# Optimization experiments

Hardware: AMD Instinct MI355X
Metric: run time of the kernel (lower is better)

The kernel has to match this reference:

```python
import jax, jax.numpy as jnp
import numpy as np

B, N, E = 32, 128, 8192        # graphs, nodes/graph, edges total
IN, ED, H = 64, 32, 128        # node feat, edge feat, hidden
K1, K2, K3 = 64, 32, 16        # ceil(0.5*N) cascade from TopKPooling(ratio=0.5)
EPS = 1e-5


def setup_inputs():
    key = jax.random.key(0)
    ks = jax.random.split(key, 20)
    def rn(i, shape, s=1.0):
        return jax.random.normal(ks[i], shape, dtype=jnp.float32) * s
    x = rn(0, (B * N, IN))
    edge_attr = rn(1, (E, ED))
    epg = E // B  # edges per graph (intra-graph only)
    src = jax.random.randint(ks[2], (B, epg), 0, N)
    dst = jax.random.randint(ks[3], (B, epg), 0, N)
    off = (jnp.arange(B) * N)[:, None]
    edge_index = jnp.stack([(src + off).reshape(-1), (dst + off).reshape(-1)]).astype(jnp.int32)
    batch = jnp.repeat(jnp.arange(B), N).astype(jnp.int32)
    p = {}
    p['nn1_w'] = rn(4, (ED, IN * H), 0.05); p['nn1_b'] = jnp.zeros((IN * H,), jnp.float32)
    p['root1'] = rn(5, (IN, H), 0.1);       p['bias1'] = jnp.zeros((H,), jnp.float32)
    p['nn2_w'] = rn(6, (ED, H * H), 0.05);  p['nn2_b'] = jnp.zeros((H * H,), jnp.float32)
    p['root2'] = rn(7, (H, H), 0.1);        p['bias2'] = jnp.zeros((H,), jnp.float32)
    p['nn3_w'] = rn(8, (ED, H * H), 0.05);  p['nn3_b'] = jnp.zeros((H * H,), jnp.float32)
    p['root3'] = rn(9, (H, H), 0.1);        p['bias3'] = jnp.zeros((H,), jnp.float32)
    for k in ('1', '2', '3'):
        p['gamma' + k] = jnp.ones((H,), jnp.float32)
        p['beta' + k] = jnp.zeros((H,), jnp.float32)
    p['pw1'] = rn(10, (H,), 0.1); p['pw2'] = rn(11, (H,), 0.1); p['pw3'] = rn(12, (H,), 0.1)
    p['lin1_w'] = rn(13, (H, H // 2), 0.1); p['lin1_b'] = jnp.zeros((H // 2,), jnp.float32)
    p['lin2_w'] = rn(14, (H // 2, 1), 0.1); p['lin2_b'] = jnp.zeros((1,), jnp.float32)
    return dict(x=x, edge_index=edge_index, edge_attr=edge_attr, batch=batch, **p)


def _nnconv(x, src, dst, emask, eattr, nn_w, nn_b, root, bias, cin, cout, n_nodes):
    # per-edge weight matrix from edge MLP: [E, cin, cout]
    w = (eattr @ nn_w + nn_b).reshape(-1, cin, cout)
    msg = jnp.einsum('ei,eio->eo', x[src], w) * emask[:, None]  # per-edge matvec
    agg = jnp.zeros((n_nodes, cout), x.dtype).at[dst].add(msg)  # scatter-add aggr
    return agg + x @ root + bias


def _bn(x, gamma, beta):
    mu = x.mean(0)
    var = x.var(0)
    return gamma * (x - mu) * jax.lax.rsqrt(var + EPS) + beta


def _topk_pool(x, src, dst, emask, pw, nb, npg, k):
    # PyG TopKPooling: score = tanh((x.p)/||p||); keep top ceil(ratio*n) per graph
    score = jnp.tanh((x @ pw) / jnp.linalg.norm(pw))            # [nb*npg]
    _, idx = jax.lax.top_k(score.reshape(nb, npg), k)           # [nb, k]
    perm = (idx + (jnp.arange(nb) * npg)[:, None]).reshape(-1)  # global node ids
    x_new = x[perm] * score[perm][:, None]
    mapping = jnp.full((nb * npg,), -1, jnp.int32).at[perm].set(
        jnp.arange(nb * k, dtype=jnp.int32))
    ns, nd = mapping[src], mapping[dst]
    valid = (ns >= 0) & (nd >= 0) & emask   # filter_adj via mask, static shapes
    return x_new, jnp.where(valid, ns, 0), jnp.where(valid, nd, 0), valid


def _forward(x, edge_attr, nn1_w, nn1_b, root1, bias1, gamma1, beta1, pw1,
             nn2_w, nn2_b, root2, bias2, gamma2, beta2, pw2,
             nn3_w, nn3_b, root3, bias3, gamma3, beta3, pw3,
             lin1_w, lin1_b, lin2_w, lin2_b, edge_index):
    src0, dst0 = edge_index[0], edge_index[1]
    m0 = jnp.ones((E,), bool)
    h = _nnconv(x, src0, dst0, m0, edge_attr, nn1_w, nn1_b, root1, bias1, IN, H, B * N)
    h = jax.nn.relu(_bn(h, gamma1, beta1))
    h, s1, d1, m1 = _topk_pool(h, src0, dst0, m0, pw1, B, N, K1)
    h = _nnconv(h, s1, d1, m1, edge_attr, nn2_w, nn2_b, root2, bias2, H, H, B * K1)
    h = jax.nn.relu(_bn(h, gamma2, beta2))
    h, s2, d2, m2 = _topk_pool(h, s1, d1, m1, pw2, B, K1, K2)
    h = _nnconv(h, s2, d2, m2, edge_attr, nn3_w, nn3_b, root3, bias3, H, H, B * K2)
    h = jax.nn.relu(_bn(h, gamma3, beta3))
    h, _, _, _ = _topk_pool(h, s2, d2, m2, pw3, B, K2, K3)
    g = h.reshape(B, K3, H).mean(axis=1)          # global_mean_pool (equal-size graphs)
    g = jax.nn.relu(g @ lin1_w + lin1_b)          # dropout is identity in eval mode
    return jax.nn.sigmoid(g @ lin2_w + lin2_b)    # [B, 1]


def reference(x, edge_index, edge_attr, batch,
              nn1_w, nn1_b, root1, bias1, nn2_w, nn2_b, root2, bias2,
              nn3_w, nn3_b, root3, bias3, gamma1, beta1, gamma2, beta2,
              gamma3, beta3, pw1, pw2, pw3, lin1_w, lin1_b, lin2_w, lin2_b):
    return _forward(x, edge_attr, nn1_w, nn1_b, root1, bias1, gamma1, beta1, pw1,
                    nn2_w, nn2_b, root2, bias2, gamma2, beta2, pw2,
                    nn3_w, nn3_b, root3, bias3, gamma3, beta3, pw3,
                    lin1_w, lin1_b, lin2_w, lin2_b, edge_index)
```

## Files before the change

### kernel.cpp

```cpp
#include <hip/hip_runtime.h>

#define E_TOT 8192
#define NB    32
#define H     128
#define EPG   256
#define NDT   34
#define YD    33
#define YCOLS (YD * H)

typedef __attribute__((ext_vector_type(8))) short bf16x8;
typedef __attribute__((ext_vector_type(4))) float f32x4;

__device__ __forceinline__ unsigned short bf16_rne(float f) {
    unsigned int u = __float_as_uint(f);
    unsigned int r = (u + 0x7FFFu + ((u >> 16) & 1u)) >> 16;
    return (unsigned short)r;
}
__device__ __forceinline__ float bf16_to_f32(unsigned short h) {
    return __uint_as_float(((unsigned int)h) << 16);
}

__device__ __forceinline__ void gload_lds16(const void* g, void* l) {
    __builtin_amdgcn_global_load_lds(
        (const __attribute__((address_space(1))) unsigned int*)g,
        (__attribute__((address_space(3))) unsigned int*)l, 16, 0, 0);
}

template<int CIN>
__global__ __launch_bounds__(128)
void build_A(const float* __restrict__ x, unsigned short* __restrict__ A)
{
    const int v = blockIdx.x;
    unsigned short* row = A + (size_t)v * (3 * CIN);
    for (int i = threadIdx.x; i < CIN; i += 128) {
        const float val = x[(size_t)v * CIN + i];
        const unsigned short h = bf16_rne(val);
        const unsigned short l = bf16_rne(val - bf16_to_f32(h));
        row[i] = h; row[CIN + i] = h; row[2 * CIN + i] = l;
    }
}

template<int CIN>
__global__ __launch_bounds__(256)
void build_Bt(const float* __restrict__ nnw, const float* __restrict__ nnb,
              const float* __restrict__ root, unsigned short* __restrict__ Bt)
{
    const int d  = blockIdx.x;
    const int i0 = blockIdx.y * 32;
    const float* __restrict__ W =
        (d < 32) ? (nnw + (size_t)d * CIN * 128) : ((d == 32) ? nnb : root);

    __shared__ unsigned short LHI[128][40];
    __shared__ unsigned short LLO[128][40];

    for (int idx = threadIdx.x; idx < 32 * 128; idx += 256) {
        const int ii = idx >> 7, o = idx & 127;
        const float val = W[(size_t)(i0 + ii) * 128 + o];
        const unsigned short h = bf16_rne(val);
        const unsigned short l = bf16_rne(val - bf16_to_f32(h));
        LHI[o][ii] = h; LLO[o][ii] = l;
    }
    __syncthreads();

    const int o    = threadIdx.x & 127;
    const int half = threadIdx.x >> 7;
    unsigned short* dst = Bt + (size_t)(d * 128 + o) * (3 * CIN);
    const uint4* hs = (const uint4*)&LHI[o][0];
    const uint4* ls = (const uint4*)&LLO[o][0];
    if (half == 0) {
        uint4* p = (uint4*)(dst + i0);
        p[0] = hs[0]; p[1] = hs[1]; p[2] = hs[2]; p[3] = hs[3];
        uint4* q = (uint4*)(dst + 2 * CIN + i0);
        q[0] = ls[0]; q[1] = ls[1]; q[2] = ls[2]; q[3] = ls[3];
    } else {
        uint4* p = (uint4*)(dst + CIN + i0);
        p[0] = hs[0]; p[1] = hs[1]; p[2] = hs[2]; p[3] = hs[3];
    }
}

template<int K3>
__global__ __launch_bounds__(256)
void ygemm_mfma(const unsigned short* __restrict__ A,
                const unsigned short* __restrict__ Bt,
                float* __restrict__ Y,
                const float* __restrict__ bias,
                float* __restrict__ h)
{
    __shared__ unsigned short Alds[128 * 32];
    __shared__ unsigned short Blds[128 * 32];

    const int lane = threadIdx.x & 63;
    const int w    = threadIdx.x >> 6;
    const int wm = w >> 1, wn = w & 1;
    const int v0 = blockIdx.x * 128;
    const int n0 = blockIdx.y * 128;

    f32x4 acc[4][4];
    #pragma unroll
    for (int i = 0; i < 4; ++i)
        #pragma unroll
        for (int j = 0; j < 4; ++j)
            acc[i][j] = (f32x4)(0.0f);

    const int arow = lane >> 2;
    const int acol = (lane & 3) * 8;
    const int koff = (lane >> 4) * 8;
    const int mrow = lane & 15;

    for (int k0 = 0; k0 < K3; k0 += 32) {
        __syncthreads();
        #pragma unroll
        for (int t = 0; t < 2; ++t) {
            const int c = w * 2 + t;
            const int r = c * 16 + arow;
            gload_lds16(A  + (size_t)(v0 + r) * K3 + k0 + acol, &Alds[c * 512]);
            gload_lds16(Bt + (size_t)(n0 + r) * K3 + k0 + acol, &Blds[c * 512]);
        }
        __syncthreads();

        bf16x8 a[4], b[4];
        #pragma unroll
        for (int f = 0; f < 4; ++f) {
            a[f] = *(const bf16x8*)&Alds[(wm * 64 + f * 16 + mrow) * 32 + koff];
            b[f] = *(const bf16x8*)&Blds[(wn * 64 + f * 16 + mrow) * 32 + koff];
        }
        #pragma unroll
        for (int fm = 0; fm < 4; ++fm)
            #pragma unroll
            for (int fn = 0; fn < 4; ++fn)
                acc[fm][fn] = __builtin_amdgcn_mfma_f32_16x16x32_bf16(
                    a[fm], b[fn], acc[fm][fn], 0, 0, 0);
    }

    const int crow = (lane >> 4) * 4;
    const int ccol = lane & 15;
    const bool is_root = (blockIdx.y == YD);
    #pragma unroll
    for (int fm = 0; fm < 4; ++fm) {
        const int gr = v0 + wm * 64 + fm * 16 + crow;
        #pragma unroll
        for (int fn = 0; fn < 4; ++fn) {
            const int col = wn * 64 + fn * 16 + ccol;
            if (is_root) {
                const float bv = bias[col];
                #pragma unroll
                for (int r = 0; r < 4; ++r)
                    h[(size_t)(gr + r) * H + col] = acc[fm][fn][r] + bv;
            } else {
                const size_t gc = (size_t)blockIdx.y * H + col;
                #pragma unroll
                for (int r = 0; r < 4; ++r)
                    Y[(size_t)(gr + r) * YCOLS + gc] = acc[fm][fn][r];
            }
        }
    }
}

__global__ __launch_bounds__(256)
void contract_edges(const float* __restrict__ Y,
                    const float* __restrict__ ea,
                    const int*   __restrict__ esrc,
                    const int*   __restrict__ edst,
                    float*       __restrict__ agg)
{
    const int grp = threadIdx.x >> 5;
    const int l5  = threadIdx.x & 31;
    const int e   = blockIdx.x * 8 + grp;
    const int s   = esrc[e];
    if (s < 0) return;

    const float* yb  = Y + (size_t)s * YCOLS + l5 * 4;
    const float* ear = ea + (size_t)e * 32;

    float4 acc = *reinterpret_cast<const float4*>(yb + 32 * H);
    #pragma unroll 8
    for (int dd = 0; dd < 32; ++dd) {
        const float c = ear[dd];
        const float4 y = *reinterpret_cast<const float4*>(yb + dd * H);
        acc.x += c * y.x; acc.y += c * y.y; acc.z += c * y.z; acc.w += c * y.w;
    }
    float* out = agg + (size_t)edst[e] * H + l5 * 4;
    atomicAdd(out + 0, acc.x);
    atomicAdd(out + 1, acc.y);
    atomicAdd(out + 2, acc.z);
    atomicAdd(out + 3, acc.w);
}

__global__ __launch_bounds__(256)
void bn_stats(const float* __restrict__ h, int n,
              float* __restrict__ gsum, float* __restrict__ gsumsq)
{
    const int tid   = threadIdx.x;
    const int col   = tid & 127;
    const int rhalf = tid >> 7;
    float s = 0.f, sq = 0.f;
    for (int r = blockIdx.x * 2 + rhalf; r < n; r += gridDim.x * 2) {
        float v = h[(size_t)r * H + col];
        s += v; sq += v * v;
    }
    __shared__ float sh[256];
    sh[tid] = s;  __syncthreads();
    if (rhalf == 0) s += sh[tid + 128];
    __syncthreads();
    sh[tid] = sq; __syncthreads();
    if (rhalf == 0) {
        sq += sh[tid + 128];
        atomicAdd(&gsum[col], s);
        atomicAdd(&gsumsq[col], sq);
    }
}

__global__ __launch_bounds__(256)
void fused_pool(const float* __restrict__ h,
                const float* __restrict__ gsum, const float* __restrict__ gsumsq,
                float n_f,
                const float* __restrict__ gamma, const float* __restrict__ beta,
                const float* __restrict__ pw,
                int npg, int k,
                const int* __restrict__ esrc_in, const int* __restrict__ edst_in,
                int* __restrict__ esrc_out, int* __restrict__ edst_out,
                unsigned short* __restrict__ Aout)
{
    const int g   = blockIdx.x;
    const int tid = threadIdx.x;
    const int wv  = tid >> 6;
    const int ln  = tid & 63;

    __shared__ float muL[128], rsL[128], gmL[128], btL[128], pwL[128];
    __shared__ float scoreL[128], red[128];
    __shared__ int   mapL[128];
    __shared__ float sinv;

    if (tid < 128) {
        const float mu  = gsum[tid] / n_f;
        const float var = gsumsq[tid] / n_f - mu * mu;
        muL[tid] = mu;
        rsL[tid] = rsqrtf(var + 1e-5f);
        gmL[tid] = gamma[tid];
        btL[tid] = beta[tid];
        const float p = pw[tid];
        pwL[tid] = p;
        red[tid] = p * p;
    }
    __syncthreads();
    for (int off = 64; off > 0; off >>= 1) {
        if (tid < off) red[tid] += red[tid + off];
        __syncthreads();
    }
    if (tid == 0) sinv = rsqrtf(red[0]);
    __syncthreads();

    for (int r = wv; r < npg; r += 4) {
        const float* hr = h + (size_t)(g * npg + r) * H;
        float p = 0.f;
        #pragma unroll
        for (int half = 0; half < 2; ++half) {
            const int c = ln + half * 64;
            const float y = fmaxf(gmL[c] * (hr[c] - muL[c]) * rsL[c] + btL[c], 0.f);
            p += y * pwL[c];
        }
        #pragma unroll
        for (int off = 32; off > 0; off >>= 1)
            p += __shfl_down(p, off, 64);
        if (ln == 0) scoreL[r] = tanhf(p * sinv);
    }
    __syncthreads();

    if (tid < npg) {
        const float si = scoreL[tid];
        int cnt = 0;
        for (int j = 0; j < npg; ++j) {
            const float sj = scoreL[j];
            cnt += (sj > si) || (sj == si && j < tid);
        }
        mapL[tid] = (cnt < k) ? cnt : -1;
    }
    __syncthreads();

    for (int r = wv; r < npg; r += 4) {
        const int nr = mapL[r];
        if (nr < 0) continue;
        const float sc = scoreL[r];
        const float* hr = h + (size_t)(g * npg + r) * H;
        unsigned short* arow = Aout + (size_t)(g * k + nr) * 384;
        #pragma unroll
        for (int half = 0; half < 2; ++half) {
            const int c = ln + half * 64;
            const float y = fmaxf(gmL[c] * (hr[c] - muL[c]) * rsL[c] + btL[c], 0.f) * sc;
            const unsigned short hb = bf16_rne(y);
            const unsigned short lb = bf16_rne(y - bf16_to_f32(hb));
            arow[c] = hb; arow[128 + c] = hb; arow[256 + c] = lb;
        }
    }

    {
        const int e = g * EPG + tid;
        const int s = esrc_in[e];
        int ns = -1, nd = -1;
        if (s >= 0) {
            const int ms = mapL[s - g * npg];
            const int md = mapL[edst_in[e] - g * npg];
            if (ms >= 0 && md >= 0) { ns = g * k + ms; nd = g * k + md; }
        }
        esrc_out[e] = ns; edst_out[e] = nd;
    }
}

__global__ __launch_bounds__(256)
void fused_pool_final(const float* __restrict__ h,
                      const float* __restrict__ gsum, const float* __restrict__ gsumsq,
                      float n_f,
                      const float* __restrict__ gamma, const float* __restrict__ beta,
                      const float* __restrict__ pw,
                      const float* __restrict__ lin1_w, const float* __restrict__ lin1_b,
                      const float* __restrict__ lin2_w, const float* __restrict__ lin2_b,
                      float* __restrict__ out)
{
    const int g   = blockIdx.x;
    const int tid = threadIdx.x;
    const int wv  = tid >> 6;
    const int ln  = tid & 63;
    const int npg = 32, k = 16;

    __shared__ float muL[128], rsL[128], gmL[128], btL[128], pwL[128];
    __shared__ float scoreL[32], red[128], gmean[128], h1c[64];
    __shared__ int   mapL[32];
    __shared__ float sinv;

    if (tid < 128) {
        const float mu  = gsum[tid] / n_f;
        const float var = gsumsq[tid] / n_f - mu * mu;
        muL[tid] = mu;
        rsL[tid] = rsqrtf(var + 1e-5f);
        gmL[tid] = gamma[tid];
        btL[tid] = beta[tid];
        const float p = pw[tid];
        pwL[tid] = p;
        red[tid] = p * p;
    }
    __syncthreads();
    for (int off = 64; off > 0; off >>= 1) {
        if (tid < off) red[tid] += red[tid + off];
        __syncthreads();
    }
    if (tid == 0) sinv = rsqrtf(red[0]);
    __syncthreads();

    for (int r = wv; r < npg; r += 4) {
        const float* hr = h + (size_t)(g * npg + r) * H;
        float p = 0.f;
        #pragma unroll
        for (int half = 0; half < 2; ++half) {
            const int c = ln + half * 64;
            const float y = fmaxf(gmL[c] * (hr[c] - muL[c]) * rsL[c] + btL[c], 0.f);
            p += y * pwL[c];
        }
        #pragma unroll
        for (int off = 32; off > 0; off >>= 1)
            p += __shfl_down(p, off, 64);
        if (ln == 0) scoreL[r] = tanhf(p * sinv);
    }
    __syncthreads();

    if (tid < npg) {
        const float si = scoreL[tid];
        int cnt = 0;
        for (int j = 0; j < npg; ++j) {
            const float sj = scoreL[j];
            cnt += (sj > si) || (sj == si && j < tid);
        }
        mapL[tid] = (cnt < k) ? cnt : -1;
    }
    __syncthreads();

    if (tid < 128) {
        float acc = 0.f;
        for (int r = 0; r < npg; ++r) {
            if (mapL[r] < 0) continue;
            const float hv = h[(size_t)(g * npg + r) * H + tid];
            const float y  = fmaxf(gmL[tid] * (hv - muL[tid]) * rsL[tid] + btL[tid], 0.f);
            acc += y * scoreL[r];
        }
        gmean[tid] = acc * (1.0f / 16.0f);
    }
    __syncthreads();

    if (tid < 64) {
        float acc = lin1_b[tid];
        for (int o = 0; o < 128; ++o) acc += gmean[o] * lin1_w[o * 64 + tid];
        h1c[tid] = fmaxf(acc, 0.f);
    }
    __syncthreads();
    if (tid == 0) {
        float z = lin2_b[0];
        for (int j = 0; j < 64; ++j) z += h1c[j] * lin2_w[j];
        out[g] = 1.0f / (1.0f + expf(-z));
    }
}

extern "C" void kernel_launch(void* const* d_in, const int* in_sizes, int n_in,
                              void* d_out, int out_size, void* d_ws, size_t ws_size,
                              hipStream_t stream)
{
    const float* x        = (const float*)d_in[0];
    const int*   ei       = (const int*)  d_in[1];
    const float* eattr    = (const float*)d_in[2];
    const float* nn1_w    = (const float*)d_in[4];
    const float* nn1_b    = (const float*)d_in[5];
    const float* root1    = (const float*)d_in[6];
    const float* bias1    = (const float*)d_in[7];
    const float* nn2_w    = (const float*)d_in[8];
    const float* nn2_b    = (const float*)d_in[9];
    const float* root2    = (const float*)d_in[10];
    const float* bias2    = (const float*)d_in[11];
    const float* nn3_w    = (const float*)d_in[12];
    const float* nn3_b    = (const float*)d_in[13];
    const float* root3    = (const float*)d_in[14];
    const float* bias3    = (const float*)d_in[15];
    const float* gamma1   = (const float*)d_in[16];
    const float* beta1    = (const float*)d_in[17];
    const float* gamma2   = (const float*)d_in[18];
    const float* beta2    = (const float*)d_in[19];
    const float* gamma3   = (const float*)d_in[20];
    const float* beta3    = (const float*)d_in[21];
    const float* pw1      = (const float*)d_in[22];
    const float* pw2      = (const float*)d_in[23];
    const float* pw3      = (const float*)d_in[24];
    const float* lin1_w   = (const float*)d_in[25];
    const float* lin1_b   = (const float*)d_in[26];
    const float* lin2_w   = (const float*)d_in[27];
    const float* lin2_b   = (const float*)d_in[28];

    const int* ei_src = ei;
    const int* ei_dst = ei + E_TOT;

    char* wp = (char*)d_ws;
    auto alloc = [&](size_t bytes) { char* p = wp; wp += (bytes + 255) & ~(size_t)255; return p; };
    float* h1   = (float*)alloc(4096 * 128 * 4);
    float* h2   = (float*)alloc(2048 * 128 * 4);
    float* h3   = (float*)alloc(1024 * 128 * 4);
    int*   src1 = (int*)alloc(E_TOT * 4);
    int*   dst1 = (int*)alloc(E_TOT * 4);
    int*   src2 = (int*)alloc(E_TOT * 4);
    int*   dst2 = (int*)alloc(E_TOT * 4);
    float* stats = (float*)alloc(6 * 128 * 4);
    unsigned short* A1  = (unsigned short*)alloc((size_t)4096 * 192 * 2);
    unsigned short* A2  = (unsigned short*)alloc((size_t)2048 * 384 * 2);
    unsigned short* A3  = (unsigned short*)alloc((size_t)1024 * 384 * 2);
    unsigned short* Bt1 = (unsigned short*)alloc((size_t)4352 * 192 * 2);
    unsigned short* Bt2 = (unsigned short*)alloc((size_t)4352 * 384 * 2);
    unsigned short* Bt3 = (unsigned short*)alloc((size_t)4352 * 384 * 2);
    float* Ybuf = (float*)alloc((size_t)4096 * YCOLS * 4);

    hipMemsetAsync(stats, 0, 6 * 128 * sizeof(float), stream);

    build_Bt<64> <<<dim3(NDT, 2), 256, 0, stream>>>(nn1_w, nn1_b, root1, Bt1);
    build_Bt<128><<<dim3(NDT, 4), 256, 0, stream>>>(nn2_w, nn2_b, root2, Bt2);
    build_Bt<128><<<dim3(NDT, 4), 256, 0, stream>>>(nn3_w, nn3_b, root3, Bt3);
    build_A<64><<<4096, 128, 0, stream>>>(x, A1);

    ygemm_mfma<192><<<dim3(32, NDT), 256, 0, stream>>>(A1, Bt1, Ybuf, bias1, h1);
    contract_edges<<<E_TOT / 8, 256, 0, stream>>>(Ybuf, eattr, ei_src, ei_dst, h1);
    bn_stats<<<64, 256, 0, stream>>>(h1, 4096, stats, stats + 128);
    fused_pool<<<NB, 256, 0, stream>>>(h1, stats, stats + 128, 4096.0f,
                                       gamma1, beta1, pw1, 128, 64,
                                       ei_src, ei_dst, src1, dst1, A2);

    ygemm_mfma<384><<<dim3(16, NDT), 256, 0, stream>>>(A2, Bt2, Ybuf, bias2, h2);
    contract_edges<<<E_TOT / 8, 256, 0, stream>>>(Ybuf, eattr, src1, dst1, h2);
    bn_stats<<<64, 256, 0, stream>>>(h2, 2048, stats + 256, stats + 384);
    fused_pool<<<NB, 256, 0, stream>>>(h2, stats + 256, stats + 384, 2048.0f,
                                       gamma2, beta2, pw2, 64, 32,
                                       src1, dst1, src2, dst2, A3);

    ygemm_mfma<384><<<dim3(8, NDT), 256, 0, stream>>>(A3, Bt3, Ybuf, bias3, h3);
    contract_edges<<<E_TOT / 8, 256, 0, stream>>>(Ybuf, eattr, src2, dst2, h3);
    bn_stats<<<64, 256, 0, stream>>>(h3, 1024, stats + 512, stats + 640);
    fused_pool_final<<<NB, 256, 0, stream>>>(h3, stats + 512, stats + 640, 1024.0f,
                                             gamma3, beta3, pw3,
                                             lin1_w, lin1_b, lin2_w, lin2_b,
                                             (float*)d_out);
}
```

Measured before the change: 316.8 us.

## Fuse all GNN stages into one cooperative persistent kernel with grid syncs

Replaces the chain of about sixteen kernel launches (weight/input packing, three GEMM+edge-contract+BN+pool stages) with a single cooperative persistent kernel. The stages are separated by grid-wide barriers and work is distributed by grid-stride loops over up to 768 blocks, with shared memory unioned across phases. The aim is to remove per-launch overhead and inter-kernel gaps. In exchange it adds grid.sync costs, limits the GEMM phases to the resident block count, and keeps the multi-launch path as a fallback if the cooperative launch fails.

```diff
diff --git a/kernel.cpp b/kernel.cpp
--- a/kernel.cpp
+++ b/kernel.cpp
@@ -1,4 +1,7 @@
 #include <hip/hip_runtime.h>
+#include <hip/hip_cooperative_groups.h>
+
+namespace cg = cooperative_groups;
 
 #define E_TOT 8192
 #define NB    32
@@ -26,47 +29,43 @@
         (__attribute__((address_space(3))) unsigned int*)l, 16, 0, 0);
 }
 
+union alignas(16) SMem {
+    struct { unsigned short LHI[128][40]; unsigned short LLO[128][40]; } bt;
+    struct { unsigned short A[128 * 32]; unsigned short B[128 * 32]; } gm;
+    struct { float sh[256]; } bn;
+    struct {
+        float muL[128], rsL[128], gmL[128], btL[128], pwL[128];
+        float scoreL[128], red[128];
+        int   mapL[128];
+        float sinv;
+        float gmean[128], h1c[64];
+    } pool;
+};
+
+
 template<int CIN>
-__global__ __launch_bounds__(128)
-void build_A(const float* __restrict__ x, unsigned short* __restrict__ A)
-{
-    const int v = blockIdx.x;
-    unsigned short* row = A + (size_t)v * (3 * CIN);
-    for (int i = threadIdx.x; i < CIN; i += 128) {
-        const float val = x[(size_t)v * CIN + i];
-        const unsigned short h = bf16_rne(val);
-        const unsigned short l = bf16_rne(val - bf16_to_f32(h));
-        row[i] = h; row[CIN + i] = h; row[2 * CIN + i] = l;
-    }
-}
-
-template<int CIN>
-__global__ __launch_bounds__(256)
-void build_Bt(const float* __restrict__ nnw, const float* __restrict__ nnb,
-              const float* __restrict__ root, unsigned short* __restrict__ Bt)
-{
-    const int d  = blockIdx.x;
-    const int i0 = blockIdx.y * 32;
+__device__ void bt_unit(SMem& sm, const float* __restrict__ nnw,
+                        const float* __restrict__ nnb, const float* __restrict__ root,
+                        unsigned short* __restrict__ Bt, int d, int i0)
+{
+    const int tid = threadIdx.x;
     const float* __restrict__ W =
         (d < 32) ? (nnw + (size_t)d * CIN * 128) : ((d == 32) ? nnb : root);
 
-    __shared__ unsigned short LHI[128][40];
-    __shared__ unsigned short LLO[128][40];
-
-    for (int idx = threadIdx.x; idx < 32 * 128; idx += 256) {
+    for (int idx = tid; idx < 32 * 128; idx += 256) {
         const int ii = idx >> 7, o = idx & 127;
         const float val = W[(size_t)(i0 + ii) * 128 + o];
         const unsigned short h = bf16_rne(val);
         const unsigned short l = bf16_rne(val - bf16_to_f32(h));
-        LHI[o][ii] = h; LLO[o][ii] = l;
-    }
-    __syncthreads();
-
-    const int o    = threadIdx.x & 127;
-    const int half = threadIdx.x >> 7;
+        sm.bt.LHI[o][ii] = h; sm.bt.LLO[o][ii] = l;
+    }
+    __syncthreads();
+
+    const int o    = tid & 127;
+    const int half = tid >> 7;
     unsigned short* dst = Bt + (size_t)(d * 128 + o) * (3 * CIN);
-    const uint4* hs = (const uint4*)&LHI[o][0];
-    const uint4* ls = (const uint4*)&LLO[o][0];
+    const uint4* hs = (const uint4*)&sm.bt.LHI[o][0];
+    const uint4* ls = (const uint4*)&sm.bt.LLO[o][0];
     if (half == 0) {
         uint4* p = (uint4*)(dst + i0);
         p[0] = hs[0]; p[1] = hs[1]; p[2] = hs[2]; p[3] = hs[3];
@@ -76,217 +75,217 @@
         uint4* p = (uint4*)(dst + CIN + i0);
         p[0] = hs[0]; p[1] = hs[1]; p[2] = hs[2]; p[3] = hs[3];
     }
+    __syncthreads();
 }
 
 template<int K3>
-__global__ __launch_bounds__(256)
-void ygemm_mfma(const unsigned short* __restrict__ A,
-                const unsigned short* __restrict__ Bt,
-                float* __restrict__ Y,
-                const float* __restrict__ bias,
-                float* __restrict__ h)
-{
-    __shared__ unsigned short Alds[128 * 32];
-    __shared__ unsigned short Blds[128 * 32];
-
+__device__ void ygemm_phase(SMem& sm, int nb, int bid,
+                            const unsigned short* __restrict__ A,
+                            const unsigned short* __restrict__ Bt,
+                            float* __restrict__ Y,
+                            const float* __restrict__ bias,
+                            float* __restrict__ hout,
+                            int xblocks)
+{
     const int lane = threadIdx.x & 63;
     const int w    = threadIdx.x >> 6;
     const int wm = w >> 1, wn = w & 1;
-    const int v0 = blockIdx.x * 128;
-    const int n0 = blockIdx.y * 128;
-
-    f32x4 acc[4][4];
-    #pragma unroll
-    for (int i = 0; i < 4; ++i)
-        #pragma unroll
-        for (int j = 0; j < 4; ++j)
-            acc[i][j] = (f32x4)(0.0f);
-
     const int arow = lane >> 2;
     const int acol = (lane & 3) * 8;
     const int koff = (lane >> 4) * 8;
     const int mrow = lane & 15;
-
-    for (int k0 = 0; k0 < K3; k0 += 32) {
-        __syncthreads();
-        #pragma unroll
-        for (int t = 0; t < 2; ++t) {
-            const int c = w * 2 + t;
-            const int r = c * 16 + arow;
-            gload_lds16(A  + (size_t)(v0 + r) * K3 + k0 + acol, &Alds[c * 512]);
-            gload_lds16(Bt + (size_t)(n0 + r) * K3 + k0 + acol, &Blds[c * 512]);
-        }
-        __syncthreads();
-
-        bf16x8 a[4], b[4];
-        #pragma unroll
-        for (int f = 0; f < 4; ++f) {
-            a[f] = *(const bf16x8*)&Alds[(wm * 64 + f * 16 + mrow) * 32 + koff];
-            b[f] = *(const bf16x8*)&Blds[(wn * 64 + f * 16 + mrow) * 32 + koff];
-        }
-        #pragma unroll
-        for (int fm = 0; fm < 4; ++fm)
-            #pragma unroll
-            for (int fn = 0; fn < 4; ++fn)
-                acc[fm][fn] = __builtin_amdgcn_mfma_f32_16x16x32_bf16(
-                    a[fm], b[fn], acc[fm][fn], 0, 0, 0);
-    }
-
     const int crow = (lane >> 4) * 4;
     const int ccol = lane & 15;
-    const bool is_root = (blockIdx.y == YD);
-    #pragma unroll
-    for (int fm = 0; fm < 4; ++fm) {
-        const int gr = v0 + wm * 64 + fm * 16 + crow;
+
+    const int total = xblocks * NDT;
+    for (int t = bid; t < total; t += nb) {
+        const int bx = t / NDT, by = t % NDT;
+        const int v0 = bx * 128, n0 = by * 128;
+
+        f32x4 acc[4][4];
         #pragma unroll
-        for (int fn = 0; fn < 4; ++fn) {
-            const int col = wn * 64 + fn * 16 + ccol;
-            if (is_root) {
-                const float bv = bias[col];
+        for (int i = 0; i < 4; ++i)
+            #pragma unroll
+            for (int j = 0; j < 4; ++j)
+                acc[i][j] = (f32x4)(0.0f);
+
+        for (int k0 = 0; k0 < K3; k0 += 32) {
+            __syncthreads();
+            #pragma unroll
+            for (int tt = 0; tt < 2; ++tt) {
+                const int c = w * 2 + tt;
+                const int r = c * 16 + arow;
+                gload_lds16(A  + (size_t)(v0 + r) * K3 + k0 + acol, &sm.gm.A[c * 512]);
+                gload_lds16(Bt + (size_t)(n0 + r) * K3 + k0 + acol, &sm.gm.B[c * 512]);
+            }
+            __syncthreads();
+
+            bf16x8 a[4], b[4];
+            #pragma unroll
+            for (int f = 0; f < 4; ++f) {
+                a[f] = *(const bf16x8*)&sm.gm.A[(wm * 64 + f * 16 + mrow) * 32 + koff];
+                b[f] = *(const bf16x8*)&sm.gm.B[(wn * 64 + f * 16 + mrow) * 32 + koff];
+            }
+            #pragma unroll
+            for (int fm = 0; fm < 4; ++fm)
                 #pragma unroll
-                for (int r = 0; r < 4; ++r)
-                    h[(size_t)(gr + r) * H + col] = acc[fm][fn][r] + bv;
-            } else {
-                const size_t gc = (size_t)blockIdx.y * H + col;
-                #pragma unroll
-                for (int r = 0; r < 4; ++r)
-                    Y[(size_t)(gr + r) * YCOLS + gc] = acc[fm][fn][r];
+                for (int fn = 0; fn < 4; ++fn)
+                    acc[fm][fn] = __builtin_amdgcn_mfma_f32_16x16x32_bf16(
+                        a[fm], b[fn], acc[fm][fn], 0, 0, 0);
+        }
+
+        const bool is_root = (by == YD);
+        #pragma unroll
+        for (int fm = 0; fm < 4; ++fm) {
+            const int gr = v0 + wm * 64 + fm * 16 + crow;
+            #pragma unroll
+            for (int fn = 0; fn < 4; ++fn) {
+                const int col = wn * 64 + fn * 16 + ccol;
+                if (is_root) {
+                    const float bv = bias[col];
+                    #pragma unroll
+                    for (int r = 0; r < 4; ++r)
+                        hout[(size_t)(gr + r) * H + col] = acc[fm][fn][r] + bv;
+                } else {
+                    const size_t gc = (size_t)by * H + col;
+                    #pragma unroll
+                    for (int r = 0; r < 4; ++r)
+                        Y[(size_t)(gr + r) * YCOLS + gc] = acc[fm][fn][r];
+                }
             }
         }
     }
 }
 
-__global__ __launch_bounds__(256)
-void contract_edges(const float* __restrict__ Y,
-                    const float* __restrict__ ea,
-                    const int*   __restrict__ esrc,
-                    const int*   __restrict__ edst,
-                    float*       __restrict__ agg)
+__device__ void contract_phase(int nb, int bid,
+                               const float* __restrict__ Y,
+                               const float* __restrict__ ea,
+                               const int*   __restrict__ esrc,
+                               const int*   __restrict__ edst,
+                               float*       __restrict__ agg)
 {
     const int grp = threadIdx.x >> 5;
     const int l5  = threadIdx.x & 31;
-    const int e   = blockIdx.x * 8 + grp;
-    const int s   = esrc[e];
-    if (s < 0) return;
-
-    const float* yb  = Y + (size_t)s * YCOLS + l5 * 4;
-    const float* ear = ea + (size_t)e * 32;
-
-    float4 acc = *reinterpret_cast<const float4*>(yb + 32 * H);
-    #pragma unroll 8
-    for (int dd = 0; dd < 32; ++dd) {
-        const float c = ear[dd];
-        const float4 y = *reinterpret_cast<const float4*>(yb + dd * H);
-        acc.x += c * y.x; acc.y += c * y.y; acc.z += c * y.z; acc.w += c * y.w;
-    }
-    float* out = agg + (size_t)edst[e] * H + l5 * 4;
-    atomicAdd(out + 0, acc.x);
-    atomicAdd(out + 1, acc.y);
-    atomicAdd(out + 2, acc.z);
-    atomicAdd(out + 3, acc.w);
-}
-
-__global__ __launch_bounds__(256)
-void bn_stats(const float* __restrict__ h, int n,
-              float* __restrict__ gsum, float* __restrict__ gsumsq)
+    for (int b = bid; b < E_TOT / 8; b += nb) {
+        const int e = b * 8 + grp;
+        const int s = esrc[e];
+        if (s >= 0) {
+            const float* yb  = Y + (size_t)s * YCOLS + l5 * 4;
+            const float* ear = ea + (size_t)e * 32;
+
+            float4 acc = *reinterpret_cast<const float4*>(yb + 32 * H);
+            #pragma unroll 8
+            for (int dd = 0; dd < 32; ++dd) {
+                const float c = ear[dd];
+                const float4 y = *reinterpret_cast<const float4*>(yb + dd * H);
+                acc.x += c * y.x; acc.y += c * y.y; acc.z += c * y.z; acc.w += c * y.w;
+            }
+            float* out = agg + (size_t)edst[e] * H + l5 * 4;
+            atomicAdd(out + 0, acc.x);
+            atomicAdd(out + 1, acc.y);
+            atomicAdd(out + 2, acc.z);
+            atomicAdd(out + 3, acc.w);
+        }
+    }
+}
+
+__device__ void bn_phase(SMem& sm, int nb, int bid,
+                         const float* __restrict__ hbuf, int n,
+                         float* __restrict__ gsum, float* __restrict__ gsumsq)
 {
     const int tid   = threadIdx.x;
     const int col   = tid & 127;
     const int rhalf = tid >> 7;
     float s = 0.f, sq = 0.f;
-    for (int r = blockIdx.x * 2 + rhalf; r < n; r += gridDim.x * 2) {
-        float v = h[(size_t)r * H + col];
+    for (int r = bid * 2 + rhalf; r < n; r += nb * 2) {
+        float v = hbuf[(size_t)r * H + col];
         s += v; sq += v * v;
     }
-    __shared__ float sh[256];
-    sh[tid] = s;  __syncthreads();
-    if (rhalf == 0) s += sh[tid + 128];
-    __syncthreads();
-    sh[tid] = sq; __syncthreads();
-    if (rhalf == 0) {
-        sq += sh[tid + 128];
+    sm.bn.sh[tid] = s;  __syncthreads();
+    if (rhalf == 0) s += sm.bn.sh[tid + 128];
+    __syncthreads();
+    sm.bn.sh[tid] = sq; __syncthreads();
+    const bool active = (bid * 2 < n);
+    if (rhalf == 0 && active) {
+        sq += sm.bn.sh[tid + 128];
         atomicAdd(&gsum[col], s);
         atomicAdd(&gsumsq[col], sq);
     }
-}
-
-__global__ __launch_bounds__(256)
-void fused_pool(const float* __restrict__ h,
-                const float* __restrict__ gsum, const float* __restrict__ gsumsq,
-                float n_f,
-                const float* __restrict__ gamma, const float* __restrict__ beta,
-                const float* __restrict__ pw,
-                int npg, int k,
-                const int* __restrict__ esrc_in, const int* __restrict__ edst_in,
-                int* __restrict__ esrc_out, int* __restrict__ edst_out,
-                unsigned short* __restrict__ Aout)
-{
-    const int g   = blockIdx.x;
+    __syncthreads();
+}
+
+__device__ void pool_phase(SMem& sm, int g,
+                           const float* __restrict__ hbuf,
+                           const float* __restrict__ gsum, const float* __restrict__ gsumsq,
+                           float n_f,
+                           const float* __restrict__ gamma, const float* __restrict__ beta,
+                           const float* __restrict__ pw,
+                           int npg, int k,
+                           const int* __restrict__ esrc_in, const int* __restrict__ edst_in,
+                           int* __restrict__ esrc_out, int* __restrict__ edst_out,
+                           unsigned short* __restrict__ Aout)
+{
     const int tid = threadIdx.x;
     const int wv  = tid >> 6;
     const int ln  = tid & 63;
-
-    __shared__ float muL[128], rsL[128], gmL[128], btL[128], pwL[128];
-    __shared__ float scoreL[128], red[128];
-    __shared__ int   mapL[128];
-    __shared__ float sinv;
+    auto& P = sm.pool;
 
     if (tid < 128) {
         const float mu  = gsum[tid] / n_f;
         const float var = gsumsq[tid] / n_f - mu * mu;
-        muL[tid] = mu;
-        rsL[tid] = rsqrtf(var + 1e-5f);
-        gmL[tid] = gamma[tid];
-        btL[tid] = beta[tid];
+        P.muL[tid] = mu;
+        P.rsL[tid] = rsqrtf(var + 1e-5f);
+        P.gmL[tid] = gamma[tid];
+        P.btL[tid] = beta[tid];
         const float p = pw[tid];
-        pwL[tid] = p;
-        red[tid] = p * p;
+        P.pwL[tid] = p;
+        P.red[tid] = p * p;
     }
     __syncthreads();
     for (int off = 64; off > 0; off >>= 1) {
-        if (tid < off) red[tid] += red[tid + off];
+        if (tid < off) P.red[tid] += P.red[tid + off];
         __syncthreads();
     }
-    if (tid == 0) sinv = rsqrtf(red[0]);
+    if (tid == 0) P.sinv = rsqrtf(P.red[0]);
     __syncthreads();
 
     for (int r = wv; r < npg; r += 4) {
-        const float* hr = h + (size_t)(g * npg + r) * H;
+        const float* hr = hbuf + (size_t)(g * npg + r) * H;
         float p = 0.f;
         #pragma unroll
         for (int half = 0; half < 2; ++half) {
             const int c = ln + half * 64;
-            const float y = fmaxf(gmL[c] * (hr[c] - muL[c]) * rsL[c] + btL[c], 0.f);
-            p += y * pwL[c];
+            const float y = fmaxf(P.gmL[c] * (hr[c] - P.muL[c]) * P.rsL[c] + P.btL[c], 0.f);
+            p += y * P.pwL[c];
         }
         #pragma unroll
         for (int off = 32; off > 0; off >>= 1)
             p += __shfl_down(p, off, 64);
-        if (ln == 0) scoreL[r] = tanhf(p * sinv);
+        if (ln == 0) P.scoreL[r] = tanhf(p * P.sinv);
     }
     __syncthreads();
 
     if (tid < npg) {
-        const float si = scoreL[tid];
+        const float si = P.scoreL[tid];
         int cnt = 0;
         for (int j = 0; j < npg; ++j) {
-            const float sj = scoreL[j];
+            const float sj = P.scoreL[j];
             cnt += (sj > si) || (sj == si && j < tid);
         }
-        mapL[tid] = (cnt < k) ? cnt : -1;
+        P.mapL[tid] = (cnt < k) ? cnt : -1;
     }
     __syncthreads();
 
     for (int r = wv; r < npg; r += 4) {
-        const int nr = mapL[r];
+        const int nr = P.mapL[r];
         if (nr < 0) continue;
-        const float sc = scoreL[r];
-        const float* hr = h + (size_t)(g * npg + r) * H;
+        const float sc = P.scoreL[r];
+        const float* hr = hbuf + (size_t)(g * npg + r) * H;
         unsigned short* arow = Aout + (size_t)(g * k + nr) * 384;
         #pragma unroll
         for (int half = 0; half < 2; ++half) {
             const int c = ln + half * 64;
-            const float y = fmaxf(gmL[c] * (hr[c] - muL[c]) * rsL[c] + btL[c], 0.f) * sc;
+            const float y = fmaxf(P.gmL[c] * (hr[c] - P.muL[c]) * P.rsL[c] + P.btL[c], 0.f) * sc;
             const unsigned short hb = bf16_rne(y);
             const unsigned short lb = bf16_rne(y - bf16_to_f32(hb));
             arow[c] = hb; arow[128 + c] = hb; arow[256 + c] = lb;
@@ -298,104 +297,254 @@
         const int s = esrc_in[e];
         int ns = -1, nd = -1;
         if (s >= 0) {
-            const int ms = mapL[s - g * npg];
-            const int md = mapL[edst_in[e] - g * npg];
+            const int ms = P.mapL[s - g * npg];
+            const int md = P.mapL[edst_in[e] - g * npg];
             if (ms >= 0 && md >= 0) { ns = g * k + ms; nd = g * k + md; }
         }
         esrc_out[e] = ns; edst_out[e] = nd;
     }
-}
-
-__global__ __launch_bounds__(256)
-void fused_pool_final(const float* __restrict__ h,
-                      const float* __restrict__ gsum, const float* __restrict__ gsumsq,
-                      float n_f,
-                      const float* __restrict__ gamma, const float* __restrict__ beta,
-                      const float* __restrict__ pw,
-                      const float* __restrict__ lin1_w, const float* __restrict__ lin1_b,
-                      const float* __restrict__ lin2_w, const float* __restrict__ lin2_b,
-                      float* __restrict__ out)
-{
-    const int g   = blockIdx.x;
+    __syncthreads();
+}
+
+__device__ void pool_final_phase(SMem& sm, int g,
+                                 const float* __restrict__ hbuf,
+                                 const float* __restrict__ gsum, const float* __restrict__ gsumsq,
+                                 float n_f,
+                                 const float* __restrict__ gamma, const float* __restrict__ beta,
+                                 const float* __restrict__ pw,
+                                 const float* __restrict__ lin1_w, const float* __restrict__ lin1_b,
+                                 const float* __restrict__ lin2_w, const float* __restrict__ lin2_b,
+                                 float* __restrict__ out)
+{
     const int tid = threadIdx.x;
     const int wv  = tid >> 6;
     const int ln  = tid & 63;
     const int npg = 32, k = 16;
-
-    __shared__ float muL[128], rsL[128], gmL[128], btL[128], pwL[128];
-    __shared__ float scoreL[32], red[128], gmean[128], h1c[64];
-    __shared__ int   mapL[32];
-    __shared__ float sinv;
+    auto& P = sm.pool;
 
     if (tid < 128) {
         const float mu  = gsum[tid] / n_f;
         const float var = gsumsq[tid] / n_f - mu * mu;
-        muL[tid] = mu;
-        rsL[tid] = rsqrtf(var + 1e-5f);
-        gmL[tid] = gamma[tid];
-        btL[tid] = beta[tid];
+        P.muL[tid] = mu;
+        P.rsL[tid] = rsqrtf(var + 1e-5f);
+        P.gmL[tid] = gamma[tid];
+        P.btL[tid] = beta[tid];
         const float p = pw[tid];
-        pwL[tid] = p;
-        red[tid] = p * p;
+        P.pwL[tid] = p;
+        P.red[tid] = p * p;
     }
     __syncthreads();
     for (int off = 64; off > 0; off >>= 1) {
-        if (tid < off) red[tid] += red[tid + off];
+        if (tid < off) P.red[tid] += P.red[tid + off];
         __syncthreads();
     }
-    if (tid == 0) sinv = rsqrtf(red[0]);
+    if (tid == 0) P.sinv = rsqrtf(P.red[0]);
     __syncthreads();
 
     for (int r = wv; r < npg; r += 4) {
-        const float* hr = h + (size_t)(g * npg + r) * H;
+        const float* hr = hbuf + (size_t)(g * npg + r) * H;
         float p = 0.f;
         #pragma unroll
         for (int half = 0; half < 2; ++half) {
             const int c = ln + half * 64;
-            const float y = fmaxf(gmL[c] * (hr[c] - muL[c]) * rsL[c] + btL[c], 0.f);
-            p += y * pwL[c];
+            const float y = fmaxf(P.gmL[c] * (hr[c] - P.muL[c]) * P.rsL[c] + P.btL[c], 0.f);
+            p += y * P.pwL[c];
         }
         #pragma unroll
         for (int off = 32; off > 0; off >>= 1)
             p += __shfl_down(p, off, 64);
-        if (ln == 0) scoreL[r] = tanhf(p * sinv);
+        if (ln == 0) P.scoreL[r] = tanhf(p * P.sinv);
     }
     __syncthreads();
 
     if (tid < npg) {
-        const float si = scoreL[tid];
+        const float si = P.scoreL[tid];
         int cnt = 0;
         for (int j = 0; j < npg; ++j) {
-            const float sj = scoreL[j];
+            const float sj = P.scoreL[j];
             cnt += (sj > si) || (sj == si && j < tid);
         }
-        mapL[tid] = (cnt < k) ? cnt : -1;
+        P.mapL[tid] = (cnt < k) ? cnt : -1;
     }
     __syncthreads();
 
     if (tid < 128) {
         float acc = 0.f;
         for (int r = 0; r < npg; ++r) {
-            if (mapL[r] < 0) continue;
-            const float hv = h[(size_t)(g * npg + r) * H + tid];
-            const float y  = fmaxf(gmL[tid] * (hv - muL[tid]) * rsL[tid] + btL[tid], 0.f);
-            acc += y * scoreL[r];
-        }
-        gmean[tid] = acc * (1.0f / 16.0f);
+            if (P.mapL[r] < 0) continue;
+            const float hv = hbuf[(size_t)(g * npg + r) * H + tid];
+            const float y  = fmaxf(P.gmL[tid] * (hv - P.muL[tid]) * P.rsL[tid] + P.btL[tid], 0.f);
+            acc += y * P.scoreL[r];
+        }
+        P.gmean[tid] = acc * (1.0f / 16.0f);
     }
     __syncthreads();
 
     if (tid < 64) {
         float acc = lin1_b[tid];
-        for (int o = 0; o < 128; ++o) acc += gmean[o] * lin1_w[o * 64 + tid];
-        h1c[tid] = fmaxf(acc, 0.f);
+        for (int o = 0; o < 128; ++o) acc += P.gmean[o] * lin1_w[o * 64 + tid];
+        P.h1c[tid] = fmaxf(acc, 0.f);
     }
     __syncthreads();
     if (tid == 0) {
         float z = lin2_b[0];
-        for (int j = 0; j < 64; ++j) z += h1c[j] * lin2_w[j];
+        for (int j = 0; j < 64; ++j) z += P.h1c[j] * lin2_w[j];
         out[g] = 1.0f / (1.0f + expf(-z));
     }
+}
+
+struct KParams {
+    const float *x, *eattr;
+    const int *ei_src, *ei_dst;
+    const float *nn1_w, *nn1_b, *root1, *bias1;
+    const float *nn2_w, *nn2_b, *root2, *bias2;
+    const float *nn3_w, *nn3_b, *root3, *bias3;
+    const float *gamma1, *beta1, *gamma2, *beta2, *gamma3, *beta3;
+    const float *pw1, *pw2, *pw3;
+    const float *lin1_w, *lin1_b, *lin2_w, *lin2_b;
+    float *h1, *h2, *h3, *stats, *Y;
+    int *src1, *dst1, *src2, *dst2;
+    unsigned short *A1, *A2, *A3, *Bt1, *Bt2, *Bt3;
+    float *out;
+};
+
+__global__ __launch_bounds__(256, 3)
+void mega(KParams p)
+{
+    cg::grid_group grid = cg::this_grid();
+    __shared__ SMem sm;
+    const int nb  = (int)gridDim.x;
+    const int bid = (int)blockIdx.x;
+    const int tid = (int)threadIdx.x;
+
+    for (int u = bid; u < 340; u += nb) {
+        if (u < 68)       bt_unit<64 >(sm, p.nn1_w, p.nn1_b, p.root1, p.Bt1, u >> 1, (u & 1) * 32);
+        else if (u < 204) { const int t = u - 68;  bt_unit<128>(sm, p.nn2_w, p.nn2_b, p.root2, p.Bt2, t >> 2, (t & 3) * 32); }
+        else              { const int t = u - 204; bt_unit<128>(sm, p.nn3_w, p.nn3_b, p.root3, p.Bt3, t >> 2, (t & 3) * 32); }
+    }
+    for (int idx = bid * 256 + tid; idx < 4096 * 64; idx += nb * 256) {
+        const int v = idx >> 6, i = idx & 63;
+        const float val = p.x[idx];
+        const unsigned short h = bf16_rne(val);
+        const unsigned short l = bf16_rne(val - bf16_to_f32(h));
+        unsigned short* row = p.A1 + (size_t)v * 192;
+        row[i] = h; row[64 + i] = h; row[128 + i] = l;
+    }
+    for (int idx = bid * 256 + tid; idx < 6 * 128; idx += nb * 256) p.stats[idx] = 0.f;
+    grid.sync();
+
+    ygemm_phase<192>(sm, nb, bid, p.A1, p.Bt1, p.Y, p.bias1, p.h1, 32);
+    grid.sync();
+    contract_phase(nb, bid, p.Y, p.eattr, p.ei_src, p.ei_dst, p.h1);
+    grid.sync();
+    bn_phase(sm, nb, bid, p.h1, 4096, p.stats, p.stats + 128);
+    grid.sync();
+    if (bid < NB)
+        pool_phase(sm, bid, p.h1, p.stats, p.stats + 128, 4096.0f,
+                   p.gamma1, p.beta1, p.pw1, 128, 64,
+                   p.ei_src, p.ei_dst, p.src1, p.dst1, p.A2);
+    grid.sync();
+
+    ygemm_phase<384>(sm, nb, bid, p.A2, p.Bt2, p.Y, p.bias2, p.h2, 16);
+    grid.sync();
+    contract_phase(nb, bid, p.Y, p.eattr, p.src1, p.dst1, p.h2);
+    grid.sync();
+    bn_phase(sm, nb, bid, p.h2, 2048, p.stats + 256, p.stats + 384);
+    grid.sync();
+    if (bid < NB)
+        pool_phase(sm, bid, p.h2, p.stats + 256, p.stats + 384, 2048.0f,
+                   p.gamma2, p.beta2, p.pw2, 64, 32,
+                   p.src1, p.dst1, p.src2, p.dst2, p.A3);
+    grid.sync();
+
+    ygemm_phase<384>(sm, nb, bid, p.A3, p.Bt3, p.Y, p.bias3, p.h3, 8);
+    grid.sync();
+    contract_phase(nb, bid, p.Y, p.eattr, p.src2, p.dst2, p.h3);
+    grid.sync();
+    bn_phase(sm, nb, bid, p.h3, 1024, p.stats + 512, p.stats + 640);
+    grid.sync();
+    if (bid < NB)
+        pool_final_phase(sm, bid, p.h3, p.stats + 512, p.stats + 640, 1024.0f,
+                         p.gamma3, p.beta3, p.pw3,
+                         p.lin1_w, p.lin1_b, p.lin2_w, p.lin2_b, p.out);
+}
+
+template<int CIN>
+__global__ __launch_bounds__(128)
+void build_A(const float* __restrict__ x, unsigned short* __restrict__ A)
+{
+    const int v = blockIdx.x;
+    unsigned short* row = A + (size_t)v * (3 * CIN);
+    for (int i = threadIdx.x; i < CIN; i += 128) {
+        const float val = x[(size_t)v * CIN + i];
+        const unsigned short h = bf16_rne(val);
+        const unsigned short l = bf16_rne(val - bf16_to_f32(h));
+        row[i] = h; row[CIN + i] = h; row[2 * CIN + i] = l;
+    }
+}
+
+template<int CIN>
+__global__ __launch_bounds__(256)
+void build_Bt(const float* __restrict__ nnw, const float* __restrict__ nnb,
+              const float* __restrict__ root, unsigned short* __restrict__ Bt)
+{
+    __shared__ SMem sm;
+    bt_unit<CIN>(sm, nnw, nnb, root, Bt, blockIdx.x, blockIdx.y * 32);
+}
+
+template<int K3>
+__global__ __launch_bounds__(256)
+void ygemm_k(const unsigned short* __restrict__ A, const unsigned short* __restrict__ Bt,
+             float* __restrict__ Y, const float* __restrict__ bias, float* __restrict__ h,
+             int xblocks)
+{
+    __shared__ SMem sm;
+    const int t = blockIdx.x;
+    ygemm_phase<K3>(sm, xblocks * NDT, t, A, Bt, Y, bias, h, xblocks);
+}
+
+__global__ __launch_bounds__(256)
+void contract_k(const float* __restrict__ Y, const float* __restrict__ ea,
+                const int* __restrict__ esrc, const int* __restrict__ edst,
+                float* __restrict__ agg)
+{
+    contract_phase(E_TOT / 8, blockIdx.x, Y, ea, esrc, edst, agg);
+}
+
+__global__ __launch_bounds__(256)
+void bn_k(const float* __restrict__ h, int n, float* __restrict__ gsum,
+          float* __restrict__ gsumsq)
+{
+    __shared__ SMem sm;
+    bn_phase(sm, gridDim.x, blockIdx.x, h, n, gsum, gsumsq);
+}
+
+__global__ __launch_bounds__(256)
+void pool_k(const float* __restrict__ h, const float* __restrict__ gsum,
+            const float* __restrict__ gsumsq, float n_f,
+            const float* __restrict__ gamma, const float* __restrict__ beta,
+            const float* __restrict__ pw, int npg, int k,
+            const int* __restrict__ esrc_in, const int* __restrict__ edst_in,
+            int* __restrict__ esrc_out, int* __restrict__ edst_out,
+            unsigned short* __restrict__ Aout)
+{
+    __shared__ SMem sm;
+    pool_phase(sm, blockIdx.x, h, gsum, gsumsq, n_f, gamma, beta, pw, npg, k,
+               esrc_in, edst_in, esrc_out, edst_out, Aout);
+}
+
+__global__ __launch_bounds__(256)
+void pool_final_k(const float* __restrict__ h, const float* __restrict__ gsum,
+                  const float* __restrict__ gsumsq, float n_f,
+                  const float* __restrict__ gamma, const float* __restrict__ beta,
+                  const float* __restrict__ pw,
+                  const float* __restrict__ lin1_w, const float* __restrict__ lin1_b,
+                  const float* __restrict__ lin2_w, const float* __restrict__ lin2_b,
+                  float* __restrict__ out)
+{
+    __shared__ SMem sm;
+    pool_final_phase(sm, blockIdx.x, h, gsum, gsumsq, n_f, gamma, beta, pw,
+                     lin1_w, lin1_b, lin2_w, lin2_b, out);
 }
 
 extern "C" void kernel_launch(void* const* d_in, const int* in_sizes, int n_in,
@@ -452,6 +601,38 @@
     unsigned short* Bt3 = (unsigned short*)alloc((size_t)4352 * 384 * 2);
     float* Ybuf = (float*)alloc((size_t)4096 * YCOLS * 4);
 
+    static int s_grid = -1;
+    if (s_grid < 0) {
+        int mb = 0;
+        if (hipOccupancyMaxActiveBlocksPerMultiprocessor(&mb, mega, 256, 0) != hipSuccess)
+            mb = 0;
+        int g = mb * 256;
+        if (g > 768) g = 768;
+        s_grid = (g >= 64) ? g : 0;
+    }
+
+    if (s_grid > 0) {
+        KParams hp;
+        hp.x = x; hp.eattr = eattr; hp.ei_src = ei_src; hp.ei_dst = ei_dst;
+        hp.nn1_w = nn1_w; hp.nn1_b = nn1_b; hp.root1 = root1; hp.bias1 = bias1;
+        hp.nn2_w = nn2_w; hp.nn2_b = nn2_b; hp.root2 = root2; hp.bias2 = bias2;
+        hp.nn3_w = nn3_w; hp.nn3_b = nn3_b; hp.root3 = root3; hp.bias3 = bias3;
+        hp.gamma1 = gamma1; hp.beta1 = beta1; hp.gamma2 = gamma2; hp.beta2 = beta2;
+        hp.gamma3 = gamma3; hp.beta3 = beta3;
+        hp.pw1 = pw1; hp.pw2 = pw2; hp.pw3 = pw3;
+        hp.lin1_w = lin1_w; hp.lin1_b = lin1_b; hp.lin2_w = lin2_w; hp.lin2_b = lin2_b;
+        hp.h1 = h1; hp.h2 = h2; hp.h3 = h3; hp.stats = stats; hp.Y = Ybuf;
+        hp.src1 = src1; hp.dst1 = dst1; hp.src2 = src2; hp.dst2 = dst2;
+        hp.A1 = A1; hp.A2 = A2; hp.A3 = A3; hp.Bt1 = Bt1; hp.Bt2 = Bt2; hp.Bt3 = Bt3;
+        hp.out = (float*)d_out;
+
+        void* args[] = { &hp };
+        hipError_t e = hipLaunchCooperativeKernel(mega, dim3(s_grid), dim3(256),
+                                                  args, 0, stream);
+        if (e == hipSuccess) return;
+        s_grid = 0;
+    }
+
     hipMemsetAsync(stats, 0, 6 * 128 * sizeof(float), stream);
 
     build_Bt<64> <<<dim3(NDT, 2), 256, 0, stream>>>(nn1_w, nn1_b, root1, Bt1);
@@ -459,25 +640,25 @@
     build_Bt<128><<<dim3(NDT, 4), 256, 0, stream>>>(nn3_w, nn3_b, root3, Bt3);
     build_A<64><<<4096, 128, 0, stream>>>(x, A1);
 
-    ygemm_mfma<192><<<dim3(32, NDT), 256, 0, stream>>>(A1, Bt1, Ybuf, bias1, h1);
-    contract_edges<<<E_TOT / 8, 256, 0, stream>>>(Ybuf, eattr, ei_src, ei_dst, h1);
-    bn_stats<<<64, 256, 0, stream>>>(h1, 4096, stats, stats + 128);
-    fused_pool<<<NB, 256, 0, stream>>>(h1, stats, stats + 128, 4096.0f,
-                                       gamma1, beta1, pw1, 128, 64,
-                                       ei_src, ei_dst, src1, dst1, A2);
-
-    ygemm_mfma<384><<<dim3(16, NDT), 256, 0, stream>>>(A2, Bt2, Ybuf, bias2, h2);
-    contract_edges<<<E_TOT / 8, 256, 0, stream>>>(Ybuf, eattr, src1, dst1, h2);
-    bn_stats<<<64, 256, 0, stream>>>(h2, 2048, stats + 256, stats + 384);
-    fused_pool<<<NB, 256, 0, stream>>>(h2, stats + 256, stats + 384, 2048.0f,
-                                       gamma2, beta2, pw2, 64, 32,
-                                       src1, dst1, src2, dst2, A3);
-
-    ygemm_mfma<384><<<dim3(8, NDT), 256, 0, stream>>>(A3, Bt3, Ybuf, bias3, h3);
-    contract_edges<<<E_TOT / 8, 256, 0, stream>>>(Ybuf, eattr, src2, dst2, h3);
-    bn_stats<<<64, 256, 0, stream>>>(h3, 1024, stats + 512, stats + 640);
-    fused_pool_final<<<NB, 256, 0, stream>>>(h3, stats + 512, stats + 640, 1024.0f,
-                                             gamma3, beta3, pw3,
-                                             lin1_w, lin1_b, lin2_w, lin2_b,
-                                             (float*)d_out);
-}
+    ygemm_k<192><<<32 * NDT, 256, 0, stream>>>(A1, Bt1, Ybuf, bias1, h1, 32);
+    contract_k<<<E_TOT / 8, 256, 0, stream>>>(Ybuf, eattr, ei_src, ei_dst, h1);
+    bn_k<<<64, 256, 0, stream>>>(h1, 4096, stats, stats + 128);
+    pool_k<<<NB, 256, 0, stream>>>(h1, stats, stats + 128, 4096.0f,
+                                   gamma1, beta1, pw1, 128, 64,
+                                   ei_src, ei_dst, src1, dst1, A2);
+
+    ygemm_k<384><<<16 * NDT, 256, 0, stream>>>(A2, Bt2, Ybuf, bias2, h2, 16);
+    contract_k<<<E_TOT / 8, 256, 0, stream>>>(Ybuf, eattr, src1, dst1, h2);
+    bn_k<<<64, 256, 0, stream>>>(h2, 2048, stats + 256, stats + 384);
+    pool_k<<<NB, 256, 0, stream>>>(h2, stats + 256, stats + 384, 2048.0f,
+                                   gamma2, beta2, pw2, 64, 32,
+                                   src1, dst1, src2, dst2, A3);
+
+    ygemm_k<384><<<8 * NDT, 256, 0, stream>>>(A3, Bt3, Ybuf, bias3, h3, 8);
+    contract_k<<<E_TOT / 8, 256, 0, stream>>>(Ybuf, eattr, src2, dst2, h3);
+    bn_k<<<64, 256, 0, stream>>>(h3, 1024, stats + 512, stats + 640);
+    pool_final_k<<<NB, 256, 0, stream>>>(h3, stats + 512, stats + 640, 1024.0f,
+                                         gamma3, beta3, pw3,
+                                         lin1_w, lin1_b, lin2_w, lin2_b,
+                                         (float*)d_out);
+}
```

Result: slower. 335.3 us (+5.8%).

## Fuse stage-1 edge-weight GEMM with per-edge contraction in shared memory

Applied to the files above, without the earlier changes.

Replaces the stage-1 GEMM plus contract_edges pair with one kernel per graph and column chunk. Each block computes the Y tiles in registers, stages them in shared memory, and scatters edge contributions into a shared-memory aggregate with LDS atomics. It then atomically adds the result into h1, which is now zeroed with a memset. This removes the large Ybuf round trip through global memory. In exchange the grid is only 256 blocks of one wave-group each, with heavy LDS use and serialized edge atomics.

```diff
diff --git a/kernel.cpp b/kernel.cpp
--- a/kernel.cpp
+++ b/kernel.cpp
@@ -75,6 +75,134 @@
     } else {
         uint4* p = (uint4*)(dst + CIN + i0);
         p[0] = hs[0]; p[1] = hs[1]; p[2] = hs[2]; p[3] = hs[3];
+    }
+}
+
+union YS1 {
+    unsigned short stg[2][128 * 32];
+    float ytile[128][132];
+};
+
+__global__ __launch_bounds__(256, 1)
+void fused_stage1(const unsigned short* __restrict__ A,
+                  const unsigned short* __restrict__ Bt,
+                  const float* __restrict__ ea,
+                  const int*   __restrict__ esrc,
+                  const int*   __restrict__ edst,
+                  const float* __restrict__ bias,
+                  float*       __restrict__ hout)
+{
+    constexpr int K3 = 192;
+    __shared__ YS1  ys;
+    __shared__ float agg[128][132];
+
+    const int g   = blockIdx.x;
+    const int c   = blockIdx.y;
+    const int tid = threadIdx.x;
+    const int lane = tid & 63;
+    const int w    = tid >> 6;
+    const int wm = w >> 1, wn = w & 1;
+    const int arow = lane >> 2;
+    const int acol = (lane & 3) * 8;
+    const int koff = (lane >> 4) * 8;
+    const int mrow = lane & 15;
+    const int crow = (lane >> 4) * 4;
+    const int ccol = lane & 15;
+    const int v0 = g * 128;
+
+    for (int idx = tid; idx < 128 * 132; idx += 256)
+        (&agg[0][0])[idx] = 0.f;
+
+    const int jb = (c < 2) ? c * 5 : 10 + (c - 2) * 4;
+    const int je = jb + ((c < 2) ? 5 : 4);
+
+    for (int d = jb; d < je; ++d) {
+        const int n0 = d * 128;
+
+        f32x4 acc[4][4];
+        #pragma unroll
+        for (int i = 0; i < 4; ++i)
+            #pragma unroll
+            for (int j = 0; j < 4; ++j)
+                acc[i][j] = (f32x4)(0.0f);
+
+        for (int k0 = 0; k0 < K3; k0 += 32) {
+            __syncthreads();
+            #pragma unroll
+            for (int tt = 0; tt < 2; ++tt) {
+                const int cc = w * 2 + tt;
+                const int r = cc * 16 + arow;
+                gload_lds16(A  + (size_t)(v0 + r) * K3 + k0 + acol, &ys.stg[0][cc * 512]);
+                gload_lds16(Bt + (size_t)(n0 + r) * K3 + k0 + acol, &ys.stg[1][cc * 512]);
+            }
+            __syncthreads();
+
+            bf16x8 a[4], b[4];
+            #pragma unroll
+            for (int f = 0; f < 4; ++f) {
+                a[f] = *(const bf16x8*)&ys.stg[0][(wm * 64 + f * 16 + mrow) * 32 + koff];
+                b[f] = *(const bf16x8*)&ys.stg[1][(wn * 64 + f * 16 + mrow) * 32 + koff];
+            }
+            #pragma unroll
+            for (int fm = 0; fm < 4; ++fm)
+                #pragma unroll
+                for (int fn = 0; fn < 4; ++fn)
+                    acc[fm][fn] = __builtin_amdgcn_mfma_f32_16x16x32_bf16(
+                        a[fm], b[fn], acc[fm][fn], 0, 0, 0);
+        }
+        __syncthreads();
+
+        if (d == YD) {
+            #pragma unroll
+            for (int fm = 0; fm < 4; ++fm) {
+                const int rr = wm * 64 + fm * 16 + crow;
+                #pragma unroll
+                for (int fn = 0; fn < 4; ++fn) {
+                    const int col = wn * 64 + fn * 16 + ccol;
+                    const float bv = bias[col];
+                    #pragma unroll
+                    for (int r = 0; r < 4; ++r)
+                        agg[rr + r][col] += acc[fm][fn][r] + bv;
+                }
+            }
+            __syncthreads();
+            continue;
+        }
+
+        #pragma unroll
+        for (int fm = 0; fm < 4; ++fm) {
+            const int rr = wm * 64 + fm * 16 + crow;
+            #pragma unroll
+            for (int fn = 0; fn < 4; ++fn) {
+                const int col = wn * 64 + fn * 16 + ccol;
+                #pragma unroll
+                for (int r = 0; r < 4; ++r)
+                    ys.ytile[rr + r][col] = acc[fm][fn][r];
+            }
+        }
+        __syncthreads();
+
+        const int grp = tid >> 5;
+        const int l5  = tid & 31;
+        for (int i = grp; i < EPG; i += 8) {
+            const int e = g * EPG + i;
+            const int s = esrc[e];
+            if (s < 0) continue;
+            const int sl = s - v0;
+            const int dl = edst[e] - v0;
+            const float cf = (d == 32) ? 1.0f : ea[(size_t)e * 32 + d];
+            const float4 y = *(const float4*)&ys.ytile[sl][l5 * 4];
+            atomicAdd(&agg[dl][l5 * 4 + 0], cf * y.x);
+            atomicAdd(&agg[dl][l5 * 4 + 1], cf * y.y);
+            atomicAdd(&agg[dl][l5 * 4 + 2], cf * y.z);
+            atomicAdd(&agg[dl][l5 * 4 + 3], cf * y.w);
+        }
+        __syncthreads();
+    }
+
+    for (int idx = tid; idx < 128 * 128; idx += 256) {
+        const int r = idx >> 7, col = idx & 127;
+        atomicAdd(&hout[(size_t)(v0 + r) * H + col], agg[r][col]);
     }
 }
 
@@ -453,14 +581,15 @@
     float* Ybuf = (float*)alloc((size_t)4096 * YCOLS * 4);
 
     hipMemsetAsync(stats, 0, 6 * 128 * sizeof(float), stream);
+    hipMemsetAsync(h1, 0, 4096 * 128 * sizeof(float), stream);
 
     build_Bt<64> <<<dim3(NDT, 2), 256, 0, stream>>>(nn1_w, nn1_b, root1, Bt1);
     build_Bt<128><<<dim3(NDT, 4), 256, 0, stream>>>(nn2_w, nn2_b, root2, Bt2);
     build_Bt<128><<<dim3(NDT, 4), 256, 0, stream>>>(nn3_w, nn3_b, root3, Bt3);
     build_A<64><<<4096, 128, 0, stream>>>(x, A1);
 
-    ygemm_mfma<192><<<dim3(32, NDT), 256, 0, stream>>>(A1, Bt1, Ybuf, bias1, h1);
-    contract_edges<<<E_TOT / 8, 256, 0, stream>>>(Ybuf, eattr, ei_src, ei_dst, h1);
+    fused_stage1<<<dim3(NB, 8), 256, 0, stream>>>(A1, Bt1, eattr, ei_src, ei_dst,
+                                                  bias1, h1);
     bn_stats<<<64, 256, 0, stream>>>(h1, 4096, stats, stats + 128);
     fused_pool<<<NB, 256, 0, stream>>>(h1, stats, stats + 128, 4096.0f,
                                        gamma1, beta1, pw1, 128, 64,
```

Result: slower. 530.2 us (+67.3%).
